# Kernel optimization log

Measured on AMD Instinct MI355X. Metric: run time of the kernel, lower is better.

## Reference

```python
import jax, jax.numpy as jnp
import numpy as np

N, F, HID, C = 8192, 256, 128, 64
ALPHA = 0.2  # LeakyReLU negative slope
NEG = -9e15  # mask value from the torch code


def xavier(key, shape, gain=1.414):
    fan_in, fan_out = shape[0], shape[1]
    limit = gain * np.sqrt(6.0 / (fan_in + fan_out))
    return jax.random.uniform(key, shape, jnp.float32, -limit, limit)


def setup_inputs() -> dict:
    key = jax.random.key(0)
    ks = jax.random.split(key, 6)
    features = jax.random.normal(ks[0], (N, F), jnp.float32)
    support = (jax.random.uniform(ks[1], (N, N)) > 0.995).astype(jnp.float32)
    support = support.at[jnp.arange(N), jnp.arange(N)].set(1.0)
    W0 = xavier(ks[2], (2 * F, HID))
    a0 = xavier(ks[3], (2 * HID, 1))
    W1 = xavier(ks[4], (2 * HID, C))
    a1 = xavier(ks[5], (2 * C, 1))
    return {"features": features, "support": support, "W0": W0, "a0": a0, "W1": W1, "a1": a1}


def gat_layer(x, adj, W, a, concat):
    # precalc=False branch: support = spmm(adj, x); cat with x
    s = adj @ x                               # (N, Fin)
    sup = jnp.concatenate([s, x], axis=1)     # (N, 2*Fin)
    h = sup @ W                               # (N, Fout)
    Fout = h.shape[1]
    # cat([h_i, h_j]) @ a == h_i @ a[:Fout] + h_j @ a[Fout:]  (same math, no N*N*2F tensor)
    src = h @ a[:Fout, 0]                     # (N,)
    dst = h @ a[Fout:, 0]                     # (N,)
    e = jax.nn.leaky_relu(src[:, None] + dst[None, :], ALPHA)  # (N, N)
    e = jnp.where(adj > 0, e, NEG)            # adjacency-masked scores
    att = jax.nn.softmax(e, axis=1)           # (N, N); dropout is identity in eval
    hp = att @ h                              # (N, Fout)
    return jax.nn.elu(hp) if concat else hp


def reference(features, support, W0, a0, W1, a1):
    x = gat_layer(features, support, W0, a0, concat=True)
    out = gat_layer(x, support, W1, a1, concat=False)
    return jax.nn.log_softmax(out, axis=1)
```

## Files before the change

kernel.cpp:

```cpp
#include <hip/hip_runtime.h>
#include <math.h>
#include <stdint.h>

#define NROWS 8192
#define EDGE_CAP 128

using f4v = __attribute__((ext_vector_type(4))) float;

__device__ __forceinline__ uint16_t bfpack(float f) {
    uint32_t x = __float_as_uint(f);
    return (uint16_t)((x + 0x7FFFu + ((x >> 16) & 1u)) >> 16);
}
__device__ __forceinline__ float bfun(uint16_t u) {
    return __uint_as_float((uint32_t)u << 16);
}

__global__ __launch_bounds__(256) void fused_csr_gemm1(const float* __restrict__ adj,
                                                       int* __restrict__ cnt,
                                                       int* __restrict__ col,
                                                       const float* __restrict__ A,
                                                       const float* __restrict__ W,
                                                       float* __restrict__ Y,
                                                       float* __restrict__ Z) {
    __shared__ float As[16][64];
    __shared__ float Bs[16][128];
    int gb  = blockIdx.x;
    int tid = threadIdx.x;

    if (gb < 256) {
        int bm = gb & 127, bn = gb >> 7;
        int tx = tid & 15, ty = tid >> 4;
        const float* Wb = W + (size_t)bn * 256 * 128;
        float acc[4][8] = {};
        for (int k0 = 0; k0 < 256; k0 += 16) {
            {
                int r = tid >> 2, kk = (tid & 3) * 4;
                float4 v = *(const float4*)&A[(size_t)(bm * 64 + r) * 256 + k0 + kk];
                As[kk + 0][r] = v.x; As[kk + 1][r] = v.y;
                As[kk + 2][r] = v.z; As[kk + 3][r] = v.w;
            }
            {
                int kk = tid >> 4, c = (tid & 15) * 8;
                *(float4*)&Bs[kk][c]     = *(const float4*)&Wb[(size_t)(k0 + kk) * 128 + c];
                *(float4*)&Bs[kk][c + 4] = *(const float4*)&Wb[(size_t)(k0 + kk) * 128 + c + 4];
            }
            __syncthreads();
            #pragma unroll
            for (int kk = 0; kk < 16; ++kk) {
                float a[4], b[8];
                #pragma unroll
                for (int i = 0; i < 4; ++i) a[i] = As[kk][ty * 4 + i];
                #pragma unroll
                for (int j = 0; j < 8; ++j) b[j] = Bs[kk][tx * 8 + j];
                #pragma unroll
                for (int i = 0; i < 4; ++i)
                    #pragma unroll
                    for (int j = 0; j < 8; ++j) acc[i][j] += a[i] * b[j];
            }
            __syncthreads();
        }
        float* O = bn ? Z : Y;
        #pragma unroll
        for (int i = 0; i < 4; ++i) {
            int r = bm * 64 + ty * 4 + i;
            float4 v0 = {acc[i][0], acc[i][1], acc[i][2], acc[i][3]};
            float4 v1 = {acc[i][4], acc[i][5], acc[i][6], acc[i][7]};
            *(float4*)&O[(size_t)r * 128 + tx * 8]     = v0;
            *(float4*)&O[(size_t)r * 128 + tx * 8 + 4] = v1;
        }
    } else {
        int row  = (gb - 256) * 4 + (tid >> 6);
        int lane = tid & 63;
        const f4v* arow = (const f4v*)(adj + (size_t)row * NROWS);
        int* crow = col + (size_t)row * EDGE_CAP;
        int count = 0;
        for (int it = 0; it < NROWS / 256; ++it) {
            f4v v = __builtin_nontemporal_load(&arow[it * 64 + lane]);
            float vv[4] = {v.x, v.y, v.z, v.w};
            #pragma unroll
            for (int p = 0; p < 4; ++p) {
                bool nz = vv[p] > 0.0f;
                unsigned long long m = __ballot(nz);
                if (nz) {
                    int off = count + __popcll(m & ((1ull << lane) - 1ull));
                    if (off < EDGE_CAP) crow[off] = it * 256 + lane * 4 + p;
                }
                count += __popcll(m);
            }
        }
        if (lane == 0) cnt[row] = count < EDGE_CAP ? count : EDGE_CAP;
    }
}

__global__ __launch_bounds__(256) void spmm_scores_128(const int* __restrict__ cnt,
                                                       const int* __restrict__ col,
                                                       const float* __restrict__ Y,
                                                       const float* __restrict__ Z,
                                                       const float* __restrict__ a,
                                                       float* __restrict__ H,
                                                       float* __restrict__ src,
                                                       float* __restrict__ dst) {
    __shared__ int sbuf[4][EDGE_CAP];
    int wav  = threadIdx.x >> 6;
    int lane = threadIdx.x & 63;
    int row  = blockIdx.x * 4 + wav;
    int n    = cnt[row];
    const int* cr = col + (size_t)row * EDGE_CAP;
    for (int e = lane; e < n; e += 64) sbuf[wav][e] = cr[e];

    const float2* Y2 = (const float2*)Y;
    float2 s = {0.0f, 0.0f};
    int e = 0;
    for (; e + 8 <= n; e += 8) {
        float2 v[8];
        #pragma unroll
        for (int u = 0; u < 8; ++u) {
            int j = sbuf[wav][e + u];
            v[u] = Y2[(size_t)j * 64 + lane];
        }
        #pragma unroll
        for (int u = 0; u < 8; ++u) { s.x += v[u].x; s.y += v[u].y; }
    }
    for (; e < n; ++e) {
        int j = sbuf[wav][e];
        float2 v = Y2[(size_t)j * 64 + lane];
        s.x += v.x; s.y += v.y;
    }
    float2 z = ((const float2*)Z)[(size_t)row * 64 + lane];
    float hx = s.x + z.x, hy = s.y + z.y;
    float2 hv = {hx, hy};
    ((float2*)H)[(size_t)row * 64 + lane] = hv;
    float s1 = hx * a[lane * 2] + hy * a[lane * 2 + 1];
    float s2 = hx * a[128 + lane * 2] + hy * a[128 + lane * 2 + 1];
    #pragma unroll
    for (int off = 32; off; off >>= 1) {
        s1 += __shfl_xor(s1, off);
        s2 += __shfl_xor(s2, off);
    }
    if (lane == 0) { src[row] = s1; dst[row] = s2; }
}

__global__ __launch_bounds__(256) void attn_agg_gemm2(const int* __restrict__ cnt,
                                                      const int* __restrict__ col,
                                                      const float* __restrict__ H,
                                                      const float* __restrict__ src,
                                                      const float* __restrict__ dst,
                                                      const float* __restrict__ W1,
                                                      float* __restrict__ Y2,
                                                      float* __restrict__ Z2) {
    __shared__ float pbuf[4][EDGE_CAP];
    __shared__ int   cbuf[4][EDGE_CAP];
    __shared__ float xrow[4][128];
    int wav  = threadIdx.x >> 6;
    int lane = threadIdx.x & 63;
    int row  = blockIdx.x * 4 + wav;
    int n    = cnt[row];
    const int* cr = col + (size_t)row * EDGE_CAP;
    float si = src[row];

    float m = -3.0e38f;
    for (int e = lane; e < n; e += 64) {
        int j = cr[e];
        float x = si + dst[j];
        x = x > 0.0f ? x : 0.2f * x;
        cbuf[wav][e] = j;
        pbuf[wav][e] = x;
        m = fmaxf(m, x);
    }
    #pragma unroll
    for (int off = 32; off; off >>= 1) m = fmaxf(m, __shfl_xor(m, off));

    float ssum = 0.0f;
    for (int e = lane; e < n; e += 64) {
        float p = __expf(pbuf[wav][e] - m);
        pbuf[wav][e] = p;
        ssum += p;
    }
    #pragma unroll
    for (int off = 32; off; off >>= 1) ssum += __shfl_xor(ssum, off);
    float inv = 1.0f / ssum;

    const float2* H2 = (const float2*)H;
    float2 o = {0.0f, 0.0f};
    int e = 0;
    for (; e + 8 <= n; e += 8) {
        float2 v[8]; float p[8];
        #pragma unroll
        for (int u = 0; u < 8; ++u) {
            int j = cbuf[wav][e + u];
            p[u] = pbuf[wav][e + u];
            v[u] = H2[(size_t)j * 64 + lane];
        }
        #pragma unroll
        for (int u = 0; u < 8; ++u) { o.x += p[u] * v[u].x; o.y += p[u] * v[u].y; }
    }
    for (; e < n; ++e) {
        int j = cbuf[wav][e];
        float p = pbuf[wav][e];
        float2 v = H2[(size_t)j * 64 + lane];
        o.x += p * v.x; o.y += p * v.y;
    }
    float vx = o.x * inv, vy = o.y * inv;
    vx = vx > 0.0f ? vx : (__expf(vx) - 1.0f);
    vy = vy > 0.0f ? vy : (__expf(vy) - 1.0f);

    float2 hv = {vx, vy};
    ((float2*)&xrow[wav][0])[lane] = hv;

    float y = 0.0f, z = 0.0f;
    #pragma unroll 8
    for (int k = 0; k < 128; ++k) {
        float xk = xrow[wav][k];
        y += xk * W1[(size_t)k * 64 + lane];
        z += xk * W1[(size_t)(128 + k) * 64 + lane];
    }
    Y2[(size_t)row * 64 + lane] = y;
    Z2[(size_t)row * 64 + lane] = z;
}

__global__ __launch_bounds__(256) void spmm_scores_64(const int* __restrict__ cnt,
                                                      const int* __restrict__ col,
                                                      const float* __restrict__ Y,
                                                      const float* __restrict__ Z,
                                                      const float* __restrict__ a,
                                                      uint16_t* __restrict__ Hb,
                                                      float* __restrict__ src,
                                                      float* __restrict__ dst) {
    __shared__ int sbuf[4][EDGE_CAP];
    int wav  = threadIdx.x >> 6;
    int lane = threadIdx.x & 63;
    int row  = blockIdx.x * 4 + wav;
    int n    = cnt[row];
    const int* cr = col + (size_t)row * EDGE_CAP;
    for (int e = lane; e < n; e += 64) sbuf[wav][e] = cr[e];

    float s = 0.0f;
    int e = 0;
    for (; e + 8 <= n; e += 8) {
        float v[8];
        #pragma unroll
        for (int u = 0; u < 8; ++u) v[u] = Y[(size_t)sbuf[wav][e + u] * 64 + lane];
        #pragma unroll
        for (int u = 0; u < 8; ++u) s += v[u];
    }
    for (; e < n; ++e) s += Y[(size_t)sbuf[wav][e] * 64 + lane];
    float h = s + Z[(size_t)row * 64 + lane];
    Hb[(size_t)row * 64 + lane] = bfpack(h);
    float s1 = h * a[lane];
    float s2 = h * a[64 + lane];
    #pragma unroll
    for (int off = 32; off; off >>= 1) {
        s1 += __shfl_xor(s1, off);
        s2 += __shfl_xor(s2, off);
    }
    if (lane == 0) { src[row] = s1; dst[row] = s2; }
}

__global__ __launch_bounds__(256) void attn_agg_final(const int* __restrict__ cnt,
                                                      const int* __restrict__ col,
                                                      const uint16_t* __restrict__ Hb,
                                                      const float* __restrict__ src,
                                                      const float* __restrict__ dst,
                                                      float* __restrict__ out) {
    __shared__ float pbuf[4][EDGE_CAP];
    __shared__ int   cbuf[4][EDGE_CAP];
    int wav  = threadIdx.x >> 6;
    int lane = threadIdx.x & 63;
    int row  = blockIdx.x * 4 + wav;
    int n    = cnt[row];
    const int* cr = col + (size_t)row * EDGE_CAP;
    float si = src[row];

    float m = -3.0e38f;
    for (int e = lane; e < n; e += 64) {
        int j = cr[e];
        float x = si + dst[j];
        x = x > 0.0f ? x : 0.2f * x;
        cbuf[wav][e] = j;
        pbuf[wav][e] = x;
        m = fmaxf(m, x);
    }
    #pragma unroll
    for (int off = 32; off; off >>= 1) m = fmaxf(m, __shfl_xor(m, off));

    float ssum = 0.0f;
    for (int e = lane; e < n; e += 64) {
        float p = __expf(pbuf[wav][e] - m);
        pbuf[wav][e] = p;
        ssum += p;
    }
    #pragma unroll
    for (int off = 32; off; off >>= 1) ssum += __shfl_xor(ssum, off);
    float inv = 1.0f / ssum;

    float o = 0.0f;
    int e = 0;
    for (; e + 8 <= n; e += 8) {
        uint16_t v[8]; float p[8];
        #pragma unroll
        for (int u = 0; u < 8; ++u) {
            p[u] = pbuf[wav][e + u];
            v[u] = Hb[(size_t)cbuf[wav][e + u] * 64 + lane];
        }
        #pragma unroll
        for (int u = 0; u < 8; ++u) o += p[u] * bfun(v[u]);
    }
    for (; e < n; ++e) o += pbuf[wav][e] * bfun(Hb[(size_t)cbuf[wav][e] * 64 + lane]);

    float logit = o * inv;
    float mm = logit;
    #pragma unroll
    for (int off = 32; off; off >>= 1) mm = fmaxf(mm, __shfl_xor(mm, off));
    float se = __expf(logit - mm);
    #pragma unroll
    for (int off = 32; off; off >>= 1) se += __shfl_xor(se, off);
    out[(size_t)row * 64 + lane] = logit - mm - logf(se);
}

extern "C" void kernel_launch(void* const* d_in, const int* in_sizes, int n_in,
                              void* d_out, int out_size, void* d_ws, size_t ws_size,
                              hipStream_t stream) {
    const float* feat = (const float*)d_in[0];
    const float* adj  = (const float*)d_in[1];
    const float* W0   = (const float*)d_in[2];
    const float* a0   = (const float*)d_in[3];
    const float* W1   = (const float*)d_in[4];
    const float* a1   = (const float*)d_in[5];
    float* out = (float*)d_out;

    char* w = (char*)d_ws;
    int* cnt      = (int*)w;        w += (size_t)NROWS * sizeof(int);
    int* col      = (int*)w;        w += (size_t)NROWS * EDGE_CAP * sizeof(int);
    float* Y1   = (float*)w;        w += (size_t)NROWS * 128 * sizeof(float);
    float* Z1   = (float*)w;        w += (size_t)NROWS * 128 * sizeof(float);
    float* H1   = (float*)w;        w += (size_t)NROWS * 128 * sizeof(float);
    float* Y2   = (float*)w;        w += (size_t)NROWS * 64 * sizeof(float);
    float* Z2   = (float*)w;        w += (size_t)NROWS * 64 * sizeof(float);
    uint16_t* H2b = (uint16_t*)w;   w += (size_t)NROWS * 64 * sizeof(uint16_t);
    float* src1 = (float*)w;        w += (size_t)NROWS * sizeof(float);
    float* dst1 = (float*)w;        w += (size_t)NROWS * sizeof(float);
    float* src2 = (float*)w;        w += (size_t)NROWS * sizeof(float);
    float* dst2 = (float*)w;        w += (size_t)NROWS * sizeof(float);

    fused_csr_gemm1<<<256 + NROWS / 4, 256, 0, stream>>>(adj, cnt, col, feat, W0, Y1, Z1);

    spmm_scores_128<<<NROWS / 4, 256, 0, stream>>>(cnt, col, Y1, Z1, a0, H1, src1, dst1);
    attn_agg_gemm2<<<NROWS / 4, 256, 0, stream>>>(cnt, col, H1, src1, dst1, W1, Y2, Z2);

    spmm_scores_64<<<NROWS / 4, 256, 0, stream>>>(cnt, col, Y2, Z2, a1, H2b, src2, dst2);
    attn_agg_final<<<NROWS / 4, 256, 0, stream>>>(cnt, col, H2b, src2, dst2, out);
}
```

Measured before the change: 432.0 us.

## Merge four per-row GAT phases into one cooperative persistent kernel with grid syncs

Replaces the four separate launches (layer-1 spmm/scores, layer-1 attention+gemm2, layer-2 spmm/scores, final attention) with one cooperative persistent kernel. Each wave walks rows in a grid-stride loop, and the phases are separated by grid-wide syncs. The aim is to remove kernel launch gaps and tail effects between the short phases. The cost is grid barrier overhead, plus occupancy now being capped by the cooperative grid size, which could cut latency hiding for the gather-heavy phases. A fallback path keeps the separate kernels in case the cooperative launch fails.

```diff
diff --git a/kernel.cpp b/kernel.cpp
--- a/kernel.cpp
+++ b/kernel.cpp
@@ -1,9 +1,12 @@
 #include <hip/hip_runtime.h>
+#include <hip/hip_cooperative_groups.h>
 #include <math.h>
 #include <stdint.h>
 
 #define NROWS 8192
 #define EDGE_CAP 128
+
+namespace cg = cooperative_groups;
 
 using f4v = __attribute__((ext_vector_type(4))) float;
 
@@ -92,79 +95,63 @@
     }
 }
 
-__global__ __launch_bounds__(256) void spmm_scores_128(const int* __restrict__ cnt,
-                                                       const int* __restrict__ col,
-                                                       const float* __restrict__ Y,
-                                                       const float* __restrict__ Z,
-                                                       const float* __restrict__ a,
-                                                       float* __restrict__ H,
-                                                       float* __restrict__ src,
-                                                       float* __restrict__ dst) {
-    __shared__ int sbuf[4][EDGE_CAP];
-    int wav  = threadIdx.x >> 6;
-    int lane = threadIdx.x & 63;
-    int row  = blockIdx.x * 4 + wav;
-    int n    = cnt[row];
+
+__device__ __forceinline__ void phaseB_row(int row, int lane, int* __restrict__ el,
+    const int* __restrict__ cnt, const int* __restrict__ col,
+    const float* __restrict__ Y1, const float* __restrict__ Z1,
+    const float* __restrict__ a0, float* __restrict__ H1,
+    float* __restrict__ src1, float* __restrict__ dst1)
+{
+    int n = cnt[row];
     const int* cr = col + (size_t)row * EDGE_CAP;
-    for (int e = lane; e < n; e += 64) sbuf[wav][e] = cr[e];
-
-    const float2* Y2 = (const float2*)Y;
+    for (int e = lane; e < n; e += 64) el[e] = cr[e];
+
+    const float2* Yv = (const float2*)Y1;
     float2 s = {0.0f, 0.0f};
     int e = 0;
     for (; e + 8 <= n; e += 8) {
         float2 v[8];
         #pragma unroll
-        for (int u = 0; u < 8; ++u) {
-            int j = sbuf[wav][e + u];
-            v[u] = Y2[(size_t)j * 64 + lane];
-        }
+        for (int u = 0; u < 8; ++u) v[u] = Yv[(size_t)el[e + u] * 64 + lane];
         #pragma unroll
         for (int u = 0; u < 8; ++u) { s.x += v[u].x; s.y += v[u].y; }
     }
     for (; e < n; ++e) {
-        int j = sbuf[wav][e];
-        float2 v = Y2[(size_t)j * 64 + lane];
+        float2 v = Yv[(size_t)el[e] * 64 + lane];
         s.x += v.x; s.y += v.y;
     }
-    float2 z = ((const float2*)Z)[(size_t)row * 64 + lane];
+    float2 z = ((const float2*)Z1)[(size_t)row * 64 + lane];
     float hx = s.x + z.x, hy = s.y + z.y;
     float2 hv = {hx, hy};
-    ((float2*)H)[(size_t)row * 64 + lane] = hv;
-    float s1 = hx * a[lane * 2] + hy * a[lane * 2 + 1];
-    float s2 = hx * a[128 + lane * 2] + hy * a[128 + lane * 2 + 1];
+    ((float2*)H1)[(size_t)row * 64 + lane] = hv;
+    float s1 = hx * a0[lane * 2] + hy * a0[lane * 2 + 1];
+    float s2 = hx * a0[128 + lane * 2] + hy * a0[128 + lane * 2 + 1];
     #pragma unroll
     for (int off = 32; off; off >>= 1) {
         s1 += __shfl_xor(s1, off);
         s2 += __shfl_xor(s2, off);
     }
-    if (lane == 0) { src[row] = s1; dst[row] = s2; }
-}
-
-__global__ __launch_bounds__(256) void attn_agg_gemm2(const int* __restrict__ cnt,
-                                                      const int* __restrict__ col,
-                                                      const float* __restrict__ H,
-                                                      const float* __restrict__ src,
-                                                      const float* __restrict__ dst,
-                                                      const float* __restrict__ W1,
-                                                      float* __restrict__ Y2,
-                                                      float* __restrict__ Z2) {
-    __shared__ float pbuf[4][EDGE_CAP];
-    __shared__ int   cbuf[4][EDGE_CAP];
-    __shared__ float xrow[4][128];
-    int wav  = threadIdx.x >> 6;
-    int lane = threadIdx.x & 63;
-    int row  = blockIdx.x * 4 + wav;
-    int n    = cnt[row];
+    if (lane == 0) { src1[row] = s1; dst1[row] = s2; }
+}
+
+__device__ __forceinline__ void phaseC_row(int row, int lane,
+    int* __restrict__ cb, float* __restrict__ pb, float* __restrict__ xr,
+    const int* __restrict__ cnt, const int* __restrict__ col,
+    const float* __restrict__ H1, const float* __restrict__ src1,
+    const float* __restrict__ dst1, const float* __restrict__ W1,
+    float* __restrict__ Y2, float* __restrict__ Z2)
+{
+    int n = cnt[row];
     const int* cr = col + (size_t)row * EDGE_CAP;
-    float si = src[row];
+    float si = src1[row];
 
     float m = -3.0e38f;
     for (int e = lane; e < n; e += 64) {
         int j = cr[e];
-        float x = si + dst[j];
+        float x = si + dst1[j];
         x = x > 0.0f ? x : 0.2f * x;
-        cbuf[wav][e] = j;
-        pbuf[wav][e] = x;
+        cb[e] = j;
+        pb[e] = x;
         m = fmaxf(m, x);
     }
     #pragma unroll
@@ -172,32 +159,30 @@
 
     float ssum = 0.0f;
     for (int e = lane; e < n; e += 64) {
-        float p = __expf(pbuf[wav][e] - m);
-        pbuf[wav][e] = p;
+        float p = __expf(pb[e] - m);
+        pb[e] = p;
         ssum += p;
     }
     #pragma unroll
     for (int off = 32; off; off >>= 1) ssum += __shfl_xor(ssum, off);
     float inv = 1.0f / ssum;
 
-    const float2* H2 = (const float2*)H;
+    const float2* Hv = (const float2*)H1;
     float2 o = {0.0f, 0.0f};
     int e = 0;
     for (; e + 8 <= n; e += 8) {
         float2 v[8]; float p[8];
         #pragma unroll
         for (int u = 0; u < 8; ++u) {
-            int j = cbuf[wav][e + u];
-            p[u] = pbuf[wav][e + u];
-            v[u] = H2[(size_t)j * 64 + lane];
+            p[u] = pb[e + u];
+            v[u] = Hv[(size_t)cb[e + u] * 64 + lane];
         }
         #pragma unroll
         for (int u = 0; u < 8; ++u) { o.x += p[u] * v[u].x; o.y += p[u] * v[u].y; }
     }
     for (; e < n; ++e) {
-        int j = cbuf[wav][e];
-        float p = pbuf[wav][e];
-        float2 v = H2[(size_t)j * 64 + lane];
+        float p = pb[e];
+        float2 v = Hv[(size_t)cb[e] * 64 + lane];
         o.x += p * v.x; o.y += p * v.y;
     }
     float vx = o.x * inv, vy = o.y * inv;
@@ -205,12 +190,12 @@
     vy = vy > 0.0f ? vy : (__expf(vy) - 1.0f);
 
     float2 hv = {vx, vy};
-    ((float2*)&xrow[wav][0])[lane] = hv;
+    ((float2*)xr)[lane] = hv;
 
     float y = 0.0f, z = 0.0f;
     #pragma unroll 8
     for (int k = 0; k < 128; ++k) {
-        float xk = xrow[wav][k];
+        float xk = xr[k];
         y += xk * W1[(size_t)k * 64 + lane];
         z += xk * W1[(size_t)(128 + k) * 64 + lane];
     }
@@ -218,66 +203,55 @@
     Z2[(size_t)row * 64 + lane] = z;
 }
 
-__global__ __launch_bounds__(256) void spmm_scores_64(const int* __restrict__ cnt,
-                                                      const int* __restrict__ col,
-                                                      const float* __restrict__ Y,
-                                                      const float* __restrict__ Z,
-                                                      const float* __restrict__ a,
-                                                      uint16_t* __restrict__ Hb,
-                                                      float* __restrict__ src,
-                                                      float* __restrict__ dst) {
-    __shared__ int sbuf[4][EDGE_CAP];
-    int wav  = threadIdx.x >> 6;
-    int lane = threadIdx.x & 63;
-    int row  = blockIdx.x * 4 + wav;
-    int n    = cnt[row];
+__device__ __forceinline__ void phaseD_row(int row, int lane, int* __restrict__ el,
+    const int* __restrict__ cnt, const int* __restrict__ col,
+    const float* __restrict__ Y2, const float* __restrict__ Z2,
+    const float* __restrict__ a1, uint16_t* __restrict__ Hb,
+    float* __restrict__ src2, float* __restrict__ dst2)
+{
+    int n = cnt[row];
     const int* cr = col + (size_t)row * EDGE_CAP;
-    for (int e = lane; e < n; e += 64) sbuf[wav][e] = cr[e];
+    for (int e = lane; e < n; e += 64) el[e] = cr[e];
 
     float s = 0.0f;
     int e = 0;
     for (; e + 8 <= n; e += 8) {
         float v[8];
         #pragma unroll
-        for (int u = 0; u < 8; ++u) v[u] = Y[(size_t)sbuf[wav][e + u] * 64 + lane];
+        for (int u = 0; u < 8; ++u) v[u] = Y2[(size_t)el[e + u] * 64 + lane];
         #pragma unroll
         for (int u = 0; u < 8; ++u) s += v[u];
     }
-    for (; e < n; ++e) s += Y[(size_t)sbuf[wav][e] * 64 + lane];
-    float h = s + Z[(size_t)row * 64 + lane];
+    for (; e < n; ++e) s += Y2[(size_t)el[e] * 64 + lane];
+    float h = s + Z2[(size_t)row * 64 + lane];
     Hb[(size_t)row * 64 + lane] = bfpack(h);
-    float s1 = h * a[lane];
-    float s2 = h * a[64 + lane];
+    float s1 = h * a1[lane];
+    float s2 = h * a1[64 + lane];
     #pragma unroll
     for (int off = 32; off; off >>= 1) {
         s1 += __shfl_xor(s1, off);
         s2 += __shfl_xor(s2, off);
     }
-    if (lane == 0) { src[row] = s1; dst[row] = s2; }
-}
-
-__global__ __launch_bounds__(256) void attn_agg_final(const int* __restrict__ cnt,
-                                                      const int* __restrict__ col,
-                                                      const uint16_t* __restrict__ Hb,
-                                                      const float* __restrict__ src,
-                                                      const float* __restrict__ dst,
-                                                      float* __restrict__ out) {
-    __shared__ float pbuf[4][EDGE_CAP];
-    __shared__ int   cbuf[4][EDGE_CAP];
-    int wav  = threadIdx.x >> 6;
-    int lane = threadIdx.x & 63;
-    int row  = blockIdx.x * 4 + wav;
-    int n    = cnt[row];
+    if (lane == 0) { src2[row] = s1; dst2[row] = s2; }
+}
+
+__device__ __forceinline__ void phaseE_row(int row, int lane,
+    int* __restrict__ cb, float* __restrict__ pb,
+    const int* __restrict__ cnt, const int* __restrict__ col,
+    const uint16_t* __restrict__ Hb, const float* __restrict__ src2,
+    const float* __restrict__ dst2, float* __restrict__ out)
+{
+    int n = cnt[row];
     const int* cr = col + (size_t)row * EDGE_CAP;
-    float si = src[row];
+    float si = src2[row];
 
     float m = -3.0e38f;
     for (int e = lane; e < n; e += 64) {
         int j = cr[e];
-        float x = si + dst[j];
+        float x = si + dst2[j];
         x = x > 0.0f ? x : 0.2f * x;
-        cbuf[wav][e] = j;
-        pbuf[wav][e] = x;
+        cb[e] = j;
+        pb[e] = x;
         m = fmaxf(m, x);
     }
     #pragma unroll
@@ -285,8 +259,8 @@
 
     float ssum = 0.0f;
     for (int e = lane; e < n; e += 64) {
-        float p = __expf(pbuf[wav][e] - m);
-        pbuf[wav][e] = p;
+        float p = __expf(pb[e] - m);
+        pb[e] = p;
         ssum += p;
     }
     #pragma unroll
@@ -299,13 +273,13 @@
         uint16_t v[8]; float p[8];
         #pragma unroll
         for (int u = 0; u < 8; ++u) {
-            p[u] = pbuf[wav][e + u];
-            v[u] = Hb[(size_t)cbuf[wav][e + u] * 64 + lane];
+            p[u] = pb[e + u];
+            v[u] = Hb[(size_t)cb[e + u] * 64 + lane];
         }
         #pragma unroll
         for (int u = 0; u < 8; ++u) o += p[u] * bfun(v[u]);
     }
-    for (; e < n; ++e) o += pbuf[wav][e] * bfun(Hb[(size_t)cbuf[wav][e] * 64 + lane]);
+    for (; e < n; ++e) o += pb[e] * bfun(Hb[(size_t)cb[e] * 64 + lane]);
 
     float logit = o * inv;
     float mm = logit;
@@ -315,6 +289,77 @@
     #pragma unroll
     for (int off = 32; off; off >>= 1) se += __shfl_xor(se, off);
     out[(size_t)row * 64 + lane] = logit - mm - logf(se);
+}
+
+__global__ __launch_bounds__(256, 4) void gat_pipeline(
+    const int* __restrict__ cnt, const int* __restrict__ col,
+    const float* __restrict__ Y1, const float* __restrict__ Z1,
+    const float* __restrict__ a0, float* __restrict__ H1,
+    float* __restrict__ src1, float* __restrict__ dst1,
+    const float* __restrict__ W1, float* __restrict__ Y2,
+    float* __restrict__ Z2, const float* __restrict__ a1,
+    uint16_t* __restrict__ Hb, float* __restrict__ src2,
+    float* __restrict__ dst2, float* __restrict__ out)
+{
+    __shared__ int   elist[4][EDGE_CAP];
+    __shared__ float pbuf[4][EDGE_CAP];
+    __shared__ float xrow[4][128];
+    const int wav  = threadIdx.x >> 6;
+    const int lane = threadIdx.x & 63;
+    const int gw   = blockIdx.x * 4 + wav;
+    const int gs   = gridDim.x * 4;
+
+    for (int row = gw; row < NROWS; row += gs)
+        phaseB_row(row, lane, elist[wav], cnt, col, Y1, Z1, a0, H1, src1, dst1);
+    __threadfence(); cg::this_grid().sync(); __threadfence();
+
+    for (int row = gw; row < NROWS; row += gs)
+        phaseC_row(row, lane, elist[wav], pbuf[wav], xrow[wav],
+                   cnt, col, H1, src1, dst1, W1, Y2, Z2);
+    __threadfence(); cg::this_grid().sync(); __threadfence();
+
+    for (int row = gw; row < NROWS; row += gs)
+        phaseD_row(row, lane, elist[wav], cnt, col, Y2, Z2, a1, Hb, src2, dst2);
+    __threadfence(); cg::this_grid().sync(); __threadfence();
+
+    for (int row = gw; row < NROWS; row += gs)
+        phaseE_row(row, lane, elist[wav], pbuf[wav], cnt, col, Hb, src2, dst2, out);
+}
+
+__global__ __launch_bounds__(256) void k_phaseB(const int* cnt, const int* col,
+    const float* Y1, const float* Z1, const float* a0,
+    float* H1, float* src1, float* dst1)
+{
+    __shared__ int elist[4][EDGE_CAP];
+    int wav = threadIdx.x >> 6, lane = threadIdx.x & 63;
+    phaseB_row(blockIdx.x * 4 + wav, lane, elist[wav], cnt, col, Y1, Z1, a0, H1, src1, dst1);
+}
+__global__ __launch_bounds__(256) void k_phaseC(const int* cnt, const int* col,
+    const float* H1, const float* src1, const float* dst1, const float* W1,
+    float* Y2, float* Z2)
+{
+    __shared__ int   cbuf[4][EDGE_CAP];
+    __shared__ float pbuf[4][EDGE_CAP];
+    __shared__ float xrow[4][128];
+    int wav = threadIdx.x >> 6, lane = threadIdx.x & 63;
+    phaseC_row(blockIdx.x * 4 + wav, lane, cbuf[wav], pbuf[wav], xrow[wav],
+               cnt, col, H1, src1, dst1, W1, Y2, Z2);
+}
+__global__ __launch_bounds__(256) void k_phaseD(const int* cnt, const int* col,
+    const float* Y2, const float* Z2, const float* a1,
+    uint16_t* Hb, float* src2, float* dst2)
+{
+    __shared__ int elist[4][EDGE_CAP];
+    int wav = threadIdx.x >> 6, lane = threadIdx.x & 63;
+    phaseD_row(blockIdx.x * 4 + wav, lane, elist[wav], cnt, col, Y2, Z2, a1, Hb, src2, dst2);
+}
+__global__ __launch_bounds__(256) void k_phaseE(const int* cnt, const int* col,
+    const uint16_t* Hb, const float* src2, const float* dst2, float* out)
+{
+    __shared__ int   cbuf[4][EDGE_CAP];
+    __shared__ float pbuf[4][EDGE_CAP];
+    int wav = threadIdx.x >> 6, lane = threadIdx.x & 63;
+    phaseE_row(blockIdx.x * 4 + wav, lane, cbuf[wav], pbuf[wav], cnt, col, Hb, src2, dst2, out);
 }
 
 extern "C" void kernel_launch(void* const* d_in, const int* in_sizes, int n_in,
@@ -326,7 +371,7 @@
     const float* a0   = (const float*)d_in[3];
     const float* W1   = (const float*)d_in[4];
     const float* a1   = (const float*)d_in[5];
-    float* out = (float*)d_out;
+    float* outp = (float*)d_out;
 
     char* w = (char*)d_ws;
     int* cnt      = (int*)w;        w += (size_t)NROWS * sizeof(int);
@@ -344,9 +389,42 @@
 
     fused_csr_gemm1<<<256 + NROWS / 4, 256, 0, stream>>>(adj, cnt, col, feat, W0, Y1, Z1);
 
-    spmm_scores_128<<<NROWS / 4, 256, 0, stream>>>(cnt, col, Y1, Z1, a0, H1, src1, dst1);
-    attn_agg_gemm2<<<NROWS / 4, 256, 0, stream>>>(cnt, col, H1, src1, dst1, W1, Y2, Z2);
-
-    spmm_scores_64<<<NROWS / 4, 256, 0, stream>>>(cnt, col, Y2, Z2, a1, H2b, src2, dst2);
-    attn_agg_final<<<NROWS / 4, 256, 0, stream>>>(cnt, col, H2b, src2, dst2, out);
-}
+    static int coop_grid = -1;
+    if (coop_grid < 0) {
+        int dev = 0;
+        (void)hipGetDevice(&dev);
+        int coopAttr = 0, nCU = 0, mb = 0;
+        (void)hipDeviceGetAttribute(&coopAttr, hipDeviceAttributeCooperativeLaunch, dev);
+        (void)hipDeviceGetAttribute(&nCU, hipDeviceAttributeMultiprocessorCount, dev);
+        hipError_t oe = hipOccupancyMaxActiveBlocksPerMultiprocessor(&mb, gat_pipeline, 256, 0);
+        if (coopAttr && oe == hipSuccess && mb > 0 && nCU > 0) {
+            long g = (long)mb * (long)nCU;
+            coop_grid = (int)(g > NROWS / 4 ? NROWS / 4 : g);
+        } else {
+            coop_grid = 0;
+        }
+    }
+
+    static bool coop_ok = true;
+    bool launched = false;
+    if (coop_grid > 0 && coop_ok) {
+        void* args[] = {(void*)&cnt, (void*)&col, (void*)&Y1, (void*)&Z1, (void*)&a0,
+                        (void*)&H1, (void*)&src1, (void*)&dst1, (void*)&W1, (void*)&Y2,
+                        (void*)&Z2, (void*)&a1, (void*)&H2b, (void*)&src2, (void*)&dst2,
+                        (void*)&outp};
+        hipError_t e = hipLaunchCooperativeKernel(gat_pipeline, dim3(coop_grid), dim3(256),
+                                                  args, 0, stream);
+        if (e == hipSuccess) {
+            launched = true;
+        } else {
+            coop_ok = false;
+            (void)hipGetLastError();
+        }
+    }
+    if (!launched) {
+        k_phaseB<<<NROWS / 4, 256, 0, stream>>>(cnt, col, Y1, Z1, a0, H1, src1, dst1);
+        k_phaseC<<<NROWS / 4, 256, 0, stream>>>(cnt, col, H1, src1, dst1, W1, Y2, Z2);
+        k_phaseD<<<NROWS / 4, 256, 0, stream>>>(cnt, col, Y2, Z2, a1, H2b, src2, dst2);
+        k_phaseE<<<NROWS / 4, 256, 0, stream>>>(cnt, col, H2b, src2, dst2, outp);
+    }
+}
```

New measurement: 865.1 us. 2x slower.
